# Kernel tuning notes

Hardware: AMD Instinct MI355X
Metric: run time of the kernel (lower is better)

Reference implementation:

```python
import jax, jax.numpy as jnp
import numpy as np

N, E, C, H = 20000, 100000, 32, 4
DH = C // H            # per-head dim (8x0e)
NB = 16                # num_basis_radial
HID = 64               # radial MLP hidden
WN = C * 1 * C         # FCTP weight numel: 32x0e (x) 1x0e -> 32x0e = 1024


def setup_inputs() -> dict:
    key = jax.random.key(0)
    ks = jax.random.split(key, 16)
    return {
        "node_features": jax.random.normal(ks[0], (N, C), jnp.float32),
        "edge_index": jax.random.randint(ks[1], (2, E), 0, N),
        "edge_sh": jax.random.normal(ks[2], (E, 1), jnp.float32),
        "edge_radial_emb": jax.random.uniform(ks[3], (E, NB), dtype=jnp.float32),
        "edge_length": jax.random.uniform(ks[4], (E, 1), dtype=jnp.float32),
        "max_radius": 1,
        # e3nn Linear / TP internal weights are N(0,1); fan-in scaling applied in forward
        "w_q": jax.random.normal(ks[5], (C, C), jnp.float32),
        "fck_w1": jax.random.normal(ks[6], (NB, HID), jnp.float32) / np.sqrt(NB),
        "fck_b1": jnp.zeros((HID,), jnp.float32),
        "fck_w2": jax.random.normal(ks[7], (HID, WN), jnp.float32) / np.sqrt(HID),
        "fck_b2": jnp.zeros((WN,), jnp.float32),
        "fcv_w1": jax.random.normal(ks[8], (NB, HID), jnp.float32) / np.sqrt(NB),
        "fcv_b1": jnp.zeros((HID,), jnp.float32),
        "fcv_w2": jax.random.normal(ks[9], (HID, WN), jnp.float32) / np.sqrt(HID),
        "fcv_b2": jnp.zeros((WN,), jnp.float32),
        "w_dot": jax.random.normal(ks[10], (DH, DH), jnp.float32),
        "w_out": jax.random.normal(ks[11], (C, C), jnp.float32),
        "ffn_w1": jax.random.normal(ks[12], (C, 2 * C), jnp.float32),
        "ffn_w2": jax.random.normal(ks[13], (2 * C, C), jnp.float32),
    }


def _radial(x, w1, b1, w2, b2):
    # RadialMLP: Linear -> SiLU -> Linear
    return jax.nn.silu(x @ w1 + b1) @ w2 + b2


def reference(node_features, edge_index, edge_sh, edge_radial_emb, edge_length,
              max_radius, w_q, fck_w1, fck_b1, fck_w2, fck_b2,
              fcv_w1, fcv_b1, fcv_w2, fcv_b2, w_dot, w_out, ffn_w1, ffn_w2):
    n = node_features.shape[0]
    e = edge_index.shape[1]
    src, dst = edge_index[0], edge_index[1]

    # query projection (e3nn Linear: weight / sqrt(fan_in))
    q = (node_features @ w_q) / np.sqrt(C)                       # (N, C)

    # edge K/V: radial-MLP-weighted fully-connected TP on scalar irreps
    x_src = node_features[src] * edge_sh                         # (E, C); sh is 1x0e
    kw = _radial(edge_radial_emb, fck_w1, fck_b1, fck_w2, fck_b2).reshape(e, C, C)
    vw = _radial(edge_radial_emb, fcv_w1, fcv_b1, fcv_w2, fcv_b2).reshape(e, C, C)
    tp_norm = 1.0 / np.sqrt(C * 1)                               # e3nn path normalization
    k_edge = jnp.einsum('ei,eik->ek', x_src, kw) * tp_norm       # (E, C)
    v_edge = jnp.einsum('ei,eik->ek', x_src, vw) * tp_norm       # (E, C)

    q_h = q.reshape(n, H, DH)[dst]                               # (E, H, DH)
    k_h = k_edge.reshape(e, H, DH)
    v_h = v_edge.reshape(e, H, DH)

    # per-head dot-product TP -> scalar; single module shared across heads
    dot_norm = 1.0 / np.sqrt(DH * DH)
    scale = 1.0 / np.sqrt(DH)
    logits = jnp.einsum('ehi,ehj,ij->eh', q_h, k_h, w_dot) * (dot_norm * scale)

    # soft radial cutoff multiplies the logits
    cutoff = jax.nn.sigmoid(10.0 * (1.0 - edge_length[:, 0] / max_radius))
    logits = logits * cutoff[:, None]

    # scatter-softmax over incoming edges per destination node
    m = jax.ops.segment_max(logits, dst, num_segments=n)         # (N, H)
    exl = jnp.exp(logits - m[dst])
    den = jax.ops.segment_sum(exl, dst, num_segments=n)
    attn = exl / den[dst]                                        # (E, H)

    agg = jax.ops.segment_sum(v_h * attn[..., None], dst, num_segments=n)  # (N,H,DH)
    out = (agg.reshape(n, C) @ w_out) / np.sqrt(C)

    attn_out = node_features + out                               # identity skip (in==out irreps)

    # FFN: Linear -> NormActivation(silu) -> Linear; for scalars: x*silu(|x|)/|x| = x*sigmoid(|x|)
    h = (attn_out @ ffn_w1) / np.sqrt(C)
    h = h * jax.nn.sigmoid(jnp.abs(h))
    ffn = (h @ ffn_w2) / np.sqrt(2 * C)

    return attn_out + ffn
```

## Files before the change

kernel.cpp:

```cpp
#include <hip/hip_runtime.h>
#include <hip/hip_bf16.h>
#include <hip/hip_fp16.h>
#include <math.h>

#define NNODE 20000
#define NEDGE 100000

typedef _Float16 f16x8 __attribute__((ext_vector_type(8)));
typedef float floatx16 __attribute__((ext_vector_type(16)));

#define OFF_FLAG 0
#define OFF_NF   64
#define OFF_SH   640064
#define OFF_CUT  740064
#define OFF_WQ   840064
#define OFF_WDOT 841088
#define OFF_WOUT 841152
#define OFF_FF1  842176
#define OFF_FF2  844224
#define OFF_BSWK 846272
#define OFF_BSWV 879040
#define OFF_BW1  911808
#define OFF_V16  912832
#define OFF_K16  2512832
#define OFF_HEAD 4112832
#define OFF_NEXT 4272832

#define RSQRT32 0.17677669529663687f
#define DOTSC   0.04419417382415922f

__device__ __forceinline__ float bf2f(unsigned short u) {
    return __uint_as_float(((unsigned)u) << 16);
}
__device__ __forceinline__ unsigned short f2h(float f) {
    return __builtin_bit_cast(unsigned short, (_Float16)f);
}
__device__ __forceinline__ _Float16 h2f16(unsigned short u) {
    return __builtin_bit_cast(_Float16, u);
}
__device__ __forceinline__ float silu(float s) {
    return s / (1.f + __expf(-s));
}

__device__ __forceinline__ unsigned detect_flag(const unsigned short* nf16) {
    __shared__ int cnt;
    if (threadIdx.x == 0) cnt = 0;
    __syncthreads();
    int c = 0;
    for (int r = 0; r < 2; ++r) {
        float v = bf2f(nf16[threadIdx.x + 256 * r]);
        float a = fabsf(v);
        if (a >= 2.44140625e-4f && a <= 32.0f) c++;
    }
    atomicAdd(&cnt, c);
    __syncthreads();
    return (cnt >= 400) ? 1u : 0u;
}

__device__ __forceinline__ float4 cvt4(const void* src, int i4, unsigned flag) {
    if (flag) {
        const uint2 u = ((const uint2*)src)[i4];
        return float4{bf2f((unsigned short)(u.x & 0xffffu)),
                      bf2f((unsigned short)(u.x >> 16)),
                      bf2f((unsigned short)(u.y & 0xffffu)),
                      bf2f((unsigned short)(u.y >> 16))};
    }
    return ((const float4*)src)[i4];
}

#define CSEG(cnt, off, srcp)                                                  \
    if (i < (cnt)) {                                                          \
        ws[(off) + i] = flag ? bf2f(((const unsigned short*)(srcp))[i])       \
                             : ((const float*)(srcp))[i];                     \
        return;                                                               \
    }                                                                         \
    i -= (cnt);

__global__ __launch_bounds__(256) void k_setup(float* __restrict__ ws,
    const void* nf, const void* sh, const void* len,
    const void* wq, const void* fk1, const void* fv1,
    const void* wdot, const void* wout, const void* ff1, const void* ff2,
    const void* fk2r, const void* fv2r) {
    const unsigned flag = detect_flag((const unsigned short*)nf);
    if (blockIdx.x == 0 && threadIdx.x == 0) ((unsigned*)ws)[0] = flag;
    int i = blockIdx.x * 256 + threadIdx.x;
    if (i < 160000) {
        ((float4*)(ws + OFF_NF))[i] = cvt4(nf, i, flag);
        return;
    }
    i -= 160000;
    if (i < 25000) {
        ((float4*)(ws + OFF_SH))[i] = cvt4(sh, i, flag);
        return;
    }
    i -= 25000;
    if (i < 25000) {
        const float4 L = cvt4(len, i, flag);
        float4 o;
        o.x = 1.f / (1.f + __expf(-10.f * (1.f - L.x)));
        o.y = 1.f / (1.f + __expf(-10.f * (1.f - L.y)));
        o.z = 1.f / (1.f + __expf(-10.f * (1.f - L.z)));
        o.w = 1.f / (1.f + __expf(-10.f * (1.f - L.w)));
        ((float4*)(ws + OFF_CUT))[i] = o;
        return;
    }
    i -= 25000;
    if (i < 40000) {
        ((int4*)((int*)ws + OFF_HEAD))[i] = int4{-1, -1, -1, -1};
        return;
    }
    i -= 40000;
    CSEG(1024, OFF_WQ,   wq)
    CSEG(64,   OFF_WDOT, wdot)
    CSEG(1024, OFF_WOUT, wout)
    CSEG(2048, OFF_FF1,  ff1)
    CSEG(2048, OFF_FF2,  ff2)
    if (i < 16384) {
        const int mlp = i >> 13, rem = i & 8191;
        const int s = rem >> 6, l = rem & 63;
        const int j = s >> 1, hf = s & 1;
        const void* w2 = mlp ? fv2r : fk2r;
        unsigned short o[8];
#pragma unroll
        for (int jj = 0; jj < 8; ++jj) {
            const int ii = hf * 16 + ((l >> 5) << 3) + jj;
            const int idx = j * 1024 + ii * 32 + (l & 31);
            const float vv = flag ? bf2f(((const unsigned short*)w2)[idx])
                                  : ((const float*)w2)[idx];
            o[jj] = f2h(vv * RSQRT32);
        }
        uint4 u;
        u.x = (unsigned)o[0] | ((unsigned)o[1] << 16);
        u.y = (unsigned)o[2] | ((unsigned)o[3] << 16);
        u.z = (unsigned)o[4] | ((unsigned)o[5] << 16);
        u.w = (unsigned)o[6] | ((unsigned)o[7] << 16);
        ((uint4*)(ws + (mlp ? OFF_BSWV : OFF_BSWK)))[s * 64 + l] = u;
        return;
    }
    i -= 16384;
    if (i < 256) {
        const int frag = i >> 6, l = i & 63;
        const int mlp = frag >> 1, nt = frag & 1;
        const void* w1 = mlp ? fv1 : fk1;
        unsigned short o[8];
#pragma unroll
        for (int jj = 0; jj < 8; ++jj) {
            const int k = ((l >> 5) << 3) + jj;
            const int idx = k * 64 + nt * 32 + (l & 31);
            const float vv = flag ? bf2f(((const unsigned short*)w1)[idx])
                                  : ((const float*)w1)[idx];
            o[jj] = f2h(vv);
        }
        uint4 u;
        u.x = (unsigned)o[0] | ((unsigned)o[1] << 16);
        u.y = (unsigned)o[2] | ((unsigned)o[3] << 16);
        u.z = (unsigned)o[4] | ((unsigned)o[5] << 16);
        u.w = (unsigned)o[6] | ((unsigned)o[7] << 16);
        ((uint4*)(ws + OFF_BW1))[frag * 64 + l] = u;
    }
}

__global__ __launch_bounds__(256, 3) void k_main(
    const float* __restrict__ ws, const void* __restrict__ emb_raw,
    const int* __restrict__ src, const int* __restrict__ dst,
    _Float16* __restrict__ v16, _Float16* __restrict__ k16,
    int* __restrict__ head, int* __restrict__ nxt) {
    __shared__ __align__(16) unsigned hw[128 * 66];
    const unsigned flag = ((const unsigned*)ws)[0];
    const int t = threadIdx.x;
    const int ebb = blockIdx.x * 128;

    if (t < 128) {
        const int e = ebb + t;
        if (e < NEDGE) nxt[e] = atomicExch(head + dst[e] * 8 + (e & 7), e);
    }

    const int w = t >> 6, lane = t & 63;
    const int hi = lane >> 5;

    {
        int ea = ebb + w * 32 + (lane & 31); if (ea >= NEDGE) ea = NEDGE - 1;
        f16x8 embA;
        if (flag) {
            const uint4 u = ((const uint4*)emb_raw)[ea * 2 + hi];
            const unsigned uu[4] = {u.x, u.y, u.z, u.w};
#pragma unroll
            for (int q = 0; q < 4; ++q) {
                embA[2 * q]     = (_Float16)bf2f((unsigned short)(uu[q] & 0xffffu));
                embA[2 * q + 1] = (_Float16)bf2f((unsigned short)(uu[q] >> 16));
            }
        } else {
            const float4* p = (const float4*)emb_raw + ea * 4 + hi * 2;
            const float4 a = p[0], b = p[1];
            embA[0] = (_Float16)a.x; embA[1] = (_Float16)a.y;
            embA[2] = (_Float16)a.z; embA[3] = (_Float16)a.w;
            embA[4] = (_Float16)b.x; embA[5] = (_Float16)b.y;
            embA[6] = (_Float16)b.z; embA[7] = (_Float16)b.w;
        }
        const uint4* bw1 = (const uint4*)(ws + OFF_BW1);
        const f16x8 bk0 = __builtin_bit_cast(f16x8, bw1[0 * 64 + lane]);
        const f16x8 bk1 = __builtin_bit_cast(f16x8, bw1[1 * 64 + lane]);
        const f16x8 bv0 = __builtin_bit_cast(f16x8, bw1[2 * 64 + lane]);
        const f16x8 bv1 = __builtin_bit_cast(f16x8, bw1[3 * 64 + lane]);
        floatx16 hk0 = {}, hk1 = {}, hv0 = {}, hv1 = {};
        hk0 = __builtin_amdgcn_mfma_f32_32x32x16_f16(embA, bk0, hk0, 0, 0, 0);
        hk1 = __builtin_amdgcn_mfma_f32_32x32x16_f16(embA, bk1, hk1, 0, 0, 0);
        hv0 = __builtin_amdgcn_mfma_f32_32x32x16_f16(embA, bv0, hv0, 0, 0, 0);
        hv1 = __builtin_amdgcn_mfma_f32_32x32x16_f16(embA, bv1, hv1, 0, 0, 0);
        const int colj = lane & 31;
#pragma unroll
        for (int r = 0; r < 16; ++r) {
            const int el = w * 32 + ((r & 3) + 8 * (r >> 2) + 4 * hi);
            hw[el * 66 + colj] =
                (unsigned)f2h(silu(hk0[r])) | ((unsigned)f2h(silu(hv0[r])) << 16);
            hw[el * 66 + 32 + colj] =
                (unsigned)f2h(silu(hk1[r])) | ((unsigned)f2h(silu(hv1[r])) << 16);
        }
    }

    const int kv = w & 1, grp = w >> 1;
    const int row = lane & 31;

    f16x8 xh[2][2];
#pragma unroll
    for (int rt = 0; rt < 2; ++rt) {
        int er = ebb + grp * 64 + rt * 32 + row; if (er >= NEDGE) er = NEDGE - 1;
        const int sn = src[er];
        const float shv = (ws + OFF_SH)[er];
        const float4* np = (const float4*)(ws + OFF_NF + sn * 32);
#pragma unroll
        for (int hf = 0; hf < 2; ++hf) {
            float4 a = np[hf * 4 + hi * 2];
            float4 b = np[hf * 4 + hi * 2 + 1];
            f16x8 x;
            x[0] = (_Float16)(a.x * shv); x[1] = (_Float16)(a.y * shv);
            x[2] = (_Float16)(a.z * shv); x[3] = (_Float16)(a.w * shv);
            x[4] = (_Float16)(b.x * shv); x[5] = (_Float16)(b.y * shv);
            x[6] = (_Float16)(b.z * shv); x[7] = (_Float16)(b.w * shv);
            xh[rt][hf] = x;
        }
    }
    __syncthreads();

    const unsigned* hb0 = hw + (grp * 64 + row) * 66;
    const unsigned* hb1 = hb0 + 32 * 66;
    const uint4* bg = (const uint4*)(ws + (kv ? OFF_BSWV : OFF_BSWK));
    floatx16 a0 = {}, a1 = {};
    const int c0 = w * 4;

#define LOADB(cc, B, H0, H1)                                                  \
    {                                                                         \
        const int c_ = (cc) & 15;                                             \
        _Pragma("unroll")                                                     \
        for (int q = 0; q < 8; ++q) B[q] = bg[(c_ * 8 + q) * 64 + lane];      \
        _Pragma("unroll")                                                     \
        for (int jl = 0; jl < 4; ++jl) {                                      \
            H0[jl] = hb0[c_ * 4 + jl];                                        \
            H1[jl] = hb1[c_ * 4 + jl];                                        \
        }                                                                     \
    }

#define DOMFMA(B, H0, H1)                                                     \
    {                                                                         \
        _Pragma("unroll")                                                     \
        for (int jl = 0; jl < 4; ++jl) {                                      \
            const unsigned h0 = H0[jl], h1 = H1[jl];                          \
            const _Float16 hr0 =                                              \
                h2f16((unsigned short)(kv ? (h0 >> 16) : (h0 & 0xffffu)));    \
            const _Float16 hr1 =                                              \
                h2f16((unsigned short)(kv ? (h1 >> 16) : (h1 & 0xffffu)));    \
            _Pragma("unroll")                                                 \
            for (int hf = 0; hf < 2; ++hf) {                                  \
                const f16x8 b = __builtin_bit_cast(f16x8, B[jl * 2 + hf]);    \
                a0 = __builtin_amdgcn_mfma_f32_32x32x16_f16(                  \
                    xh[0][hf] * hr0, b, a0, 0, 0, 0);                         \
                a1 = __builtin_amdgcn_mfma_f32_32x32x16_f16(                  \
                    xh[1][hf] * hr1, b, a1, 0, 0, 0);                         \
            }                                                                 \
        }                                                                     \
    }

    {
        uint4 bA[8], bB[8];
        unsigned hA0[4], hA1[4], hB0[4], hB1[4];
        LOADB(c0, bA, hA0, hA1);
#pragma unroll
        for (int s = 0; s < 8; ++s) {
            LOADB(c0 + 2 * s + 1, bB, hB0, hB1);
            DOMFMA(bA, hA0, hA1);
            if (s < 7) LOADB(c0 + 2 * s + 2, bA, hA0, hA1);
            DOMFMA(bB, hB0, hB1);
        }
    }
#undef LOADB
#undef DOMFMA

    _Float16* outp = kv ? v16 : k16;
    const int col = lane & 31;
#pragma unroll
    for (int rt = 0; rt < 2; ++rt) {
        const floatx16 ar = rt ? a1 : a0;
#pragma unroll
        for (int r = 0; r < 16; ++r) {
            const int rowe = (r & 3) + 8 * (r >> 2) + 4 * hi;
            const int e = ebb + grp * 64 + rt * 32 + rowe;
            if (e < NEDGE) outp[e * 32 + col] = (_Float16)ar[r];
        }
    }
}

__global__ __launch_bounds__(256) void k_final(const float* __restrict__ ws,
                                               void* __restrict__ out) {
    __shared__ float wqd[1024];
    __shared__ float s1[8][33];
    __shared__ float s_q[8][33];
    __shared__ float h_s[8][65];
    const int t = threadIdx.x, nl = t >> 5, c = t & 31, h = c >> 3;
    const int n = blockIdx.x * 8 + nl;
    const unsigned flag = ((const unsigned*)ws)[0];
    const float* cutp = ws + OFF_CUT;
    const float* wout = ws + OFF_WOUT;
    const float* ff1  = ws + OFF_FF1;
    const float* ff2  = ws + OFF_FF2;
    const _Float16* v16 = (const _Float16*)(ws + OFF_V16);
    const _Float16* k16 = (const _Float16*)(ws + OFF_K16);
    const int* headp = (const int*)ws + OFF_HEAD;
    const int* nxt   = (const int*)ws + OFF_NEXT;

    const float nfv = (ws + OFF_NF)[n * 32 + c];

    {
        const float* wqp = ws + OFF_WQ;
        const float* wd  = ws + OFF_WDOT;
        const int m0 = t >> 5, ch = t & 31, hh = ch >> 3, jx = ch & 7;
#pragma unroll
        for (int r = 0; r < 4; ++r) {
            const int m = r * 8 + m0;
            float s = 0.f;
#pragma unroll
            for (int i = 0; i < 8; ++i)
                s = fmaf(wqp[m * 32 + hh * 8 + i], wd[i * 8 + jx], s);
            wqd[m * 32 + ch] = s;
        }
    }
    s1[nl][c] = nfv;
    __syncthreads();
    {
        float s = 0.f;
#pragma unroll
        for (int m = 0; m < 32; ++m) s = fmaf(s1[nl][m], wqd[m * 32 + c], s);
        s_q[nl][c] = s * (RSQRT32 * DOTSC);
    }
    __syncthreads();

    const float q0 = s_q[nl][h * 8 + 0], q1 = s_q[nl][h * 8 + 1];
    const float q2 = s_q[nl][h * 8 + 2], q3 = s_q[nl][h * 8 + 3];
    const float q4 = s_q[nl][h * 8 + 4], q5 = s_q[nl][h * 8 + 5];
    const float q6 = s_q[nl][h * 8 + 6], q7 = s_q[nl][h * 8 + 7];

    float mm[8], dd[8], aa[8];
    int pp[8];
#pragma unroll
    for (int ch = 0; ch < 8; ++ch) {
        mm[ch] = -1e30f; dd[ch] = 0.f; aa[ch] = 0.f;
        pp[ch] = headp[8 * n + ch];
    }
    for (;;) {
        bool any = false;
#pragma unroll
        for (int ch = 0; ch < 8; ++ch) any = any || (pp[ch] >= 0);
        if (!any) break;
#pragma unroll
        for (int ch = 0; ch < 8; ++ch) {
            const int e = pp[ch];
            if (e >= 0) {
                const f16x8 kk = __builtin_bit_cast(f16x8, *(const uint4*)(k16 + e * 32 + h * 8));
                float lg = q0 * (float)kk[0] + q1 * (float)kk[1] + q2 * (float)kk[2]
                         + q3 * (float)kk[3] + q4 * (float)kk[4] + q5 * (float)kk[5]
                         + q6 * (float)kk[6] + q7 * (float)kk[7];
                lg *= cutp[e];
                const float vv = (float)v16[e * 32 + c];
                const float mn = fmaxf(mm[ch], lg);
                const float sc = __expf(mm[ch] - mn), wgt = __expf(lg - mn);
                dd[ch] = dd[ch] * sc + wgt;
                aa[ch] = aa[ch] * sc + wgt * vv;
                mm[ch] = mn;
                pp[ch] = nxt[e];
            }
        }
    }
    float mn = mm[0];
#pragma unroll
    for (int ch = 1; ch < 8; ++ch) mn = fmaxf(mn, mm[ch]);
    float dn = 0.f, acc = 0.f;
#pragma unroll
    for (int ch = 0; ch < 8; ++ch) {
        const float sc = __expf(mm[ch] - mn);
        dn += dd[ch] * sc;
        acc += aa[ch] * sc;
    }
    const float ao_in = dn > 0.f ? acc / dn : 0.f;
    __syncthreads();
    s1[nl][c] = ao_in;
    __syncthreads();
    float o = 0.f;
#pragma unroll
    for (int i2 = 0; i2 < 32; ++i2) o = fmaf(s1[nl][i2], wout[i2 * 32 + c], o);
    const float ao = nfv + o * RSQRT32;
    __syncthreads();
    s1[nl][c] = ao;
    __syncthreads();
#pragma unroll
    for (int r = 0; r < 2; ++r) {
        const int cc = c + r * 32;
        float z = 0.f;
#pragma unroll
        for (int i2 = 0; i2 < 32; ++i2) z = fmaf(s1[nl][i2], ff1[i2 * 64 + cc], z);
        z *= RSQRT32;
        z = z / (1.f + __expf(-fabsf(z)));
        h_s[nl][cc] = z;
    }
    __syncthreads();
    float f = 0.f;
#pragma unroll
    for (int i2 = 0; i2 < 64; ++i2) f = fmaf(h_s[nl][i2], ff2[i2 * 32 + c], f);
    const float fin = ao + f * 0.125f;
    if (flag) ((__hip_bfloat16*)out)[n * 32 + c] = __float2bfloat16(fin);
    else      ((float*)out)[n * 32 + c] = fin;
}

extern "C" void kernel_launch(void* const* d_in, const int* in_sizes, int n_in,
                              void* d_out, int out_size, void* d_ws, size_t ws_size,
                              hipStream_t stream) {
    (void)in_sizes; (void)n_in; (void)out_size; (void)ws_size;
    float* ws = (float*)d_ws;
    const int* eidx = (const int*)d_in[1];
    const int* src = eidx;
    const int* dst = eidx + NEDGE;

    k_setup<<<1066, 256, 0, stream>>>(ws,
        d_in[0], d_in[2], d_in[4], d_in[6], d_in[7], d_in[11],
        d_in[15], d_in[16], d_in[17], d_in[18], d_in[9], d_in[13]);
    k_main<<<(NEDGE + 127) / 128, 256, 0, stream>>>(ws, d_in[3], src, dst,
        (_Float16*)(ws + OFF_V16), (_Float16*)(ws + OFF_K16),
        (int*)ws + OFF_HEAD, (int*)ws + OFF_NEXT);
    k_final<<<NNODE / 8, 256, 0, stream>>>(ws, d_out);
}
```

Baseline: 169.3 us.

## Halve edges per block in k_main and replicate swizzled FCTP weights 8x

k_main now handles 64 edges per block instead of 128. Each wave does one 32-row MFMA tile instead of two, the LDS hidden buffer is halved, and launch bounds allow 4 blocks per CU. The swizzled K/V second-layer weights are written as 8 replicas in the workspace, and each block reads the replica chosen by blockIdx&7, to spread load contention on the shared weight table. The cost is that each weight fetch now serves half as many edges, so total weight traffic per edge doubles. Only two of the four waves run the radial first-layer MFMA, and k_setup does 8x more stores.

```diff
diff --git a/kernel.cpp b/kernel.cpp
--- a/kernel.cpp
+++ b/kernel.cpp
@@ -25,6 +25,7 @@
 #define OFF_K16  2512832
 #define OFF_HEAD 4112832
 #define OFF_NEXT 4272832
+#define OFF_BREP 4372832
 
 #define RSQRT32 0.17677669529663687f
 #define DOTSC   0.04419417382415922f
@@ -134,7 +135,10 @@
         u.y = (unsigned)o[2] | ((unsigned)o[3] << 16);
         u.z = (unsigned)o[4] | ((unsigned)o[5] << 16);
         u.w = (unsigned)o[6] | ((unsigned)o[7] << 16);
-        ((uint4*)(ws + (mlp ? OFF_BSWV : OFF_BSWK)))[s * 64 + l] = u;
+        uint4* rep = (uint4*)(ws + OFF_BREP);
+        const int idx4 = (mlp ? 8192 : 0) + s * 64 + l;
+#pragma unroll
+        for (int x = 0; x < 8; ++x) rep[x * 16384 + idx4] = u;
         return;
     }
     i -= 16384;
@@ -160,17 +164,17 @@
     }
 }
 
-__global__ __launch_bounds__(256, 3) void k_main(
+__global__ __launch_bounds__(256, 4) void k_main(
     const float* __restrict__ ws, const void* __restrict__ emb_raw,
     const int* __restrict__ src, const int* __restrict__ dst,
     _Float16* __restrict__ v16, _Float16* __restrict__ k16,
     int* __restrict__ head, int* __restrict__ nxt) {
-    __shared__ __align__(16) unsigned hw[128 * 66];
+    __shared__ __align__(16) unsigned hw[64 * 66];
     const unsigned flag = ((const unsigned*)ws)[0];
     const int t = threadIdx.x;
-    const int ebb = blockIdx.x * 128;
-
-    if (t < 128) {
+    const int ebb = blockIdx.x * 64;
+
+    if (t < 64) {
         const int e = ebb + t;
         if (e < NEDGE) nxt[e] = atomicExch(head + dst[e] * 8 + (e & 7), e);
     }
@@ -178,7 +182,7 @@
     const int w = t >> 6, lane = t & 63;
     const int hi = lane >> 5;
 
-    {
+    if (w < 2) {
         int ea = ebb + w * 32 + (lane & 31); if (ea >= NEDGE) ea = NEDGE - 1;
         f16x8 embA;
         if (flag) {
@@ -221,10 +225,9 @@
     const int kv = w & 1, grp = w >> 1;
     const int row = lane & 31;
 
-    f16x8 xh[2][2];
-#pragma unroll
-    for (int rt = 0; rt < 2; ++rt) {
-        int er = ebb + grp * 64 + rt * 32 + row; if (er >= NEDGE) er = NEDGE - 1;
+    f16x8 xh[2];
+    {
+        int er = ebb + grp * 32 + row; if (er >= NEDGE) er = NEDGE - 1;
         const int sn = src[er];
         const float shv = (ws + OFF_SH)[er];
         const float4* np = (const float4*)(ws + OFF_NF + sn * 32);
@@ -237,59 +240,52 @@
             x[2] = (_Float16)(a.z * shv); x[3] = (_Float16)(a.w * shv);
             x[4] = (_Float16)(b.x * shv); x[5] = (_Float16)(b.y * shv);
             x[6] = (_Float16)(b.z * shv); x[7] = (_Float16)(b.w * shv);
-            xh[rt][hf] = x;
-        }
-    }
-    __syncthreads();
-
-    const unsigned* hb0 = hw + (grp * 64 + row) * 66;
-    const unsigned* hb1 = hb0 + 32 * 66;
-    const uint4* bg = (const uint4*)(ws + (kv ? OFF_BSWV : OFF_BSWK));
-    floatx16 a0 = {}, a1 = {};
+            xh[hf] = x;
+        }
+    }
+    __syncthreads();
+
+    const unsigned* hb0 = hw + (grp * 32 + row) * 66;
+    const uint4* bg = (const uint4*)(ws + OFF_BREP)
+                    + (blockIdx.x & 7) * 16384 + (kv ? 8192 : 0);
+    floatx16 a0 = {};
     const int c0 = w * 4;
 
-#define LOADB(cc, B, H0, H1)                                                  \
+#define LOADB(cc, B, H0)                                                      \
     {                                                                         \
         const int c_ = (cc) & 15;                                             \
         _Pragma("unroll")                                                     \
         for (int q = 0; q < 8; ++q) B[q] = bg[(c_ * 8 + q) * 64 + lane];      \
         _Pragma("unroll")                                                     \
-        for (int jl = 0; jl < 4; ++jl) {                                      \
-            H0[jl] = hb0[c_ * 4 + jl];                                        \
-            H1[jl] = hb1[c_ * 4 + jl];                                        \
-        }                                                                     \
-    }
-
-#define DOMFMA(B, H0, H1)                                                     \
+        for (int jl = 0; jl < 4; ++jl) H0[jl] = hb0[c_ * 4 + jl];             \
+    }
+
+#define DOMFMA(B, H0)                                                         \
     {                                                                         \
         _Pragma("unroll")                                                     \
         for (int jl = 0; jl < 4; ++jl) {                                      \
-            const unsigned h0 = H0[jl], h1 = H1[jl];                          \
+            const unsigned h0 = H0[jl];                                       \
             const _Float16 hr0 =                                              \
                 h2f16((unsigned short)(kv ? (h0 >> 16) : (h0 & 0xffffu)));    \
-            const _Float16 hr1 =                                              \
-                h2f16((unsigned short)(kv ? (h1 >> 16) : (h1 & 0xffffu)));    \
             _Pragma("unroll")                                                 \
             for (int hf = 0; hf < 2; ++hf) {                                  \
                 const f16x8 b = __builtin_bit_cast(f16x8, B[jl * 2 + hf]);    \
                 a0 = __builtin_amdgcn_mfma_f32_32x32x16_f16(                  \
-                    xh[0][hf] * hr0, b, a0, 0, 0, 0);                         \
-                a1 = __builtin_amdgcn_mfma_f32_32x32x16_f16(                  \
-                    xh[1][hf] * hr1, b, a1, 0, 0, 0);                         \
+                    xh[hf] * hr0, b, a0, 0, 0, 0);                            \
             }                                                                 \
         }                                                                     \
     }
 
     {
         uint4 bA[8], bB[8];
-        unsigned hA0[4], hA1[4], hB0[4], hB1[4];
-        LOADB(c0, bA, hA0, hA1);
+        unsigned hA0[4], hB0[4];
+        LOADB(c0, bA, hA0);
 #pragma unroll
         for (int s = 0; s < 8; ++s) {
-            LOADB(c0 + 2 * s + 1, bB, hB0, hB1);
-            DOMFMA(bA, hA0, hA1);
-            if (s < 7) LOADB(c0 + 2 * s + 2, bA, hA0, hA1);
-            DOMFMA(bB, hB0, hB1);
+            LOADB(c0 + 2 * s + 1, bB, hB0);
+            DOMFMA(bA, hA0);
+            if (s < 7) LOADB(c0 + 2 * s + 2, bA, hA0);
+            DOMFMA(bB, hB0);
         }
     }
 #undef LOADB
@@ -298,14 +294,10 @@
     _Float16* outp = kv ? v16 : k16;
     const int col = lane & 31;
 #pragma unroll
-    for (int rt = 0; rt < 2; ++rt) {
-        const floatx16 ar = rt ? a1 : a0;
-#pragma unroll
-        for (int r = 0; r < 16; ++r) {
-            const int rowe = (r & 3) + 8 * (r >> 2) + 4 * hi;
-            const int e = ebb + grp * 64 + rt * 32 + rowe;
-            if (e < NEDGE) outp[e * 32 + col] = (_Float16)ar[r];
-        }
+    for (int r = 0; r < 16; ++r) {
+        const int rowe = (r & 3) + 8 * (r >> 2) + 4 * hi;
+        const int e = ebb + grp * 32 + rowe;
+        if (e < NEDGE) outp[e * 32 + col] = (_Float16)a0[r];
     }
 }
 
@@ -441,7 +433,7 @@
     k_setup<<<1066, 256, 0, stream>>>(ws,
         d_in[0], d_in[2], d_in[4], d_in[6], d_in[7], d_in[11],
         d_in[15], d_in[16], d_in[17], d_in[18], d_in[9], d_in[13]);
-    k_main<<<(NEDGE + 127) / 128, 256, 0, stream>>>(ws, d_in[3], src, dst,
+    k_main<<<(NEDGE + 63) / 64, 256, 0, stream>>>(ws, d_in[3], src, dst,
         (_Float16*)(ws + OFF_V16), (_Float16*)(ws + OFF_K16),
         (int*)ws + OFF_HEAD, (int*)ws + OFF_NEXT);
     k_final<<<NNODE / 8, 256, 0, stream>>>(ws, d_out);
```

New measurement: 173.5 us. 2.5% more time.

## Replicate swizzled MLP weights 8x and split MFMA accumulators to break dependency chains

Applied to the files above, without the earlier changes.

The prep kernel now writes eight copies of the swizzled second-layer radial weights, and each main block reads the copy selected by its block index. This is meant to spread the L2/channel traffic from all blocks loading the same weight lines. The MFMA loop also uses four independent accumulators instead of two, which shortens the dependency chains between back-to-back MFMAs, and the partial sums are added at the end. The cost is more accumulator registers, so launch bounds drop from 3 to 2 blocks per SM, plus extra workspace and extra replicated writes during prep.

```diff
diff --git a/kernel.cpp b/kernel.cpp
--- a/kernel.cpp
+++ b/kernel.cpp
@@ -25,6 +25,7 @@
 #define OFF_K16  2512832
 #define OFF_HEAD 4112832
 #define OFF_NEXT 4272832
+#define OFF_BREP 4372832
 
 #define RSQRT32 0.17677669529663687f
 #define DOTSC   0.04419417382415922f
@@ -134,7 +135,10 @@
         u.y = (unsigned)o[2] | ((unsigned)o[3] << 16);
         u.z = (unsigned)o[4] | ((unsigned)o[5] << 16);
         u.w = (unsigned)o[6] | ((unsigned)o[7] << 16);
-        ((uint4*)(ws + (mlp ? OFF_BSWV : OFF_BSWK)))[s * 64 + l] = u;
+        uint4* rep = (uint4*)(ws + OFF_BREP);
+        const int idx4 = (mlp ? 8192 : 0) + s * 64 + l;
+#pragma unroll
+        for (int x = 0; x < 8; ++x) rep[x * 16384 + idx4] = u;
         return;
     }
     i -= 16384;
@@ -160,7 +164,7 @@
     }
 }
 
-__global__ __launch_bounds__(256, 3) void k_main(
+__global__ __launch_bounds__(256, 2) void k_main(
     const float* __restrict__ ws, const void* __restrict__ emb_raw,
     const int* __restrict__ src, const int* __restrict__ dst,
     _Float16* __restrict__ v16, _Float16* __restrict__ k16,
@@ -244,8 +248,9 @@
 
     const unsigned* hb0 = hw + (grp * 64 + row) * 66;
     const unsigned* hb1 = hb0 + 32 * 66;
-    const uint4* bg = (const uint4*)(ws + (kv ? OFF_BSWV : OFF_BSWK));
-    floatx16 a0 = {}, a1 = {};
+    const uint4* bg = (const uint4*)(ws + OFF_BREP)
+                    + (blockIdx.x & 7) * 16384 + (kv ? 8192 : 0);
+    floatx16 a00 = {}, a01 = {}, a10 = {}, a11 = {};
     const int c0 = w * 4;
 
 #define LOADB(cc, B, H0, H1)                                                  \
@@ -269,14 +274,16 @@
                 h2f16((unsigned short)(kv ? (h0 >> 16) : (h0 & 0xffffu)));    \
             const _Float16 hr1 =                                              \
                 h2f16((unsigned short)(kv ? (h1 >> 16) : (h1 & 0xffffu)));    \
-            _Pragma("unroll")                                                 \
-            for (int hf = 0; hf < 2; ++hf) {                                  \
-                const f16x8 b = __builtin_bit_cast(f16x8, B[jl * 2 + hf]);    \
-                a0 = __builtin_amdgcn_mfma_f32_32x32x16_f16(                  \
-                    xh[0][hf] * hr0, b, a0, 0, 0, 0);                         \
-                a1 = __builtin_amdgcn_mfma_f32_32x32x16_f16(                  \
-                    xh[1][hf] * hr1, b, a1, 0, 0, 0);                         \
-            }                                                                 \
+            const f16x8 b0 = __builtin_bit_cast(f16x8, B[jl * 2 + 0]);        \
+            const f16x8 b1 = __builtin_bit_cast(f16x8, B[jl * 2 + 1]);        \
+            a00 = __builtin_amdgcn_mfma_f32_32x32x16_f16(                     \
+                xh[0][0] * hr0, b0, a00, 0, 0, 0);                            \
+            a10 = __builtin_amdgcn_mfma_f32_32x32x16_f16(                     \
+                xh[1][0] * hr1, b0, a10, 0, 0, 0);                            \
+            a01 = __builtin_amdgcn_mfma_f32_32x32x16_f16(                     \
+                xh[0][1] * hr0, b1, a01, 0, 0, 0);                            \
+            a11 = __builtin_amdgcn_mfma_f32_32x32x16_f16(                     \
+                xh[1][1] * hr1, b1, a11, 0, 0, 0);                            \
         }                                                                     \
     }
 
@@ -297,9 +304,10 @@
 
     _Float16* outp = kv ? v16 : k16;
     const int col = lane & 31;
+    const floatx16 accr[2] = {a00 + a01, a10 + a11};
 #pragma unroll
     for (int rt = 0; rt < 2; ++rt) {
-        const floatx16 ar = rt ? a1 : a0;
+        const floatx16 ar = accr[rt];
 #pragma unroll
         for (int r = 0; r < 16; ++r) {
             const int rowe = (r & 3) + 8 * (r >> 2) + 4 * hi;
```

Measured after the change: 172.3 us. About the same (+1.8%).

## Precompute query projection in setup and drop max-subtraction in softmax

Applied to the files above, without the earlier changes.

The query projection (node features times the fused w_q·w_dot matrix) moves out of k_final into extra threads of k_setup, which write a per-node q buffer to the workspace. Each k_final block no longer rebuilds the 32x32 fused weight in shared memory. The per-edge online softmax is replaced by a plain sum of exp(logit) with no running max, cutting one exp and the rescaling per edge. The risks are exp overflow for large logits, and redundant fused-weight recomputation in every setup thread.

```diff
diff --git a/kernel.cpp b/kernel.cpp
--- a/kernel.cpp
+++ b/kernel.cpp
@@ -13,8 +13,6 @@
 #define OFF_NF   64
 #define OFF_SH   640064
 #define OFF_CUT  740064
-#define OFF_WQ   840064
-#define OFF_WDOT 841088
 #define OFF_WOUT 841152
 #define OFF_FF1  842176
 #define OFF_FF2  844224
@@ -25,6 +23,7 @@
 #define OFF_K16  2512832
 #define OFF_HEAD 4112832
 #define OFF_NEXT 4272832
+#define OFF_Q    4372832
 
 #define RSQRT32 0.17677669529663687f
 #define DOTSC   0.04419417382415922f
@@ -55,6 +54,10 @@
     atomicAdd(&cnt, c);
     __syncthreads();
     return (cnt >= 400) ? 1u : 0u;
+}
+
+__device__ __forceinline__ float rdf(const void* p, int idx, unsigned flag) {
+    return flag ? bf2f(((const unsigned short*)p)[idx]) : ((const float*)p)[idx];
 }
 
 __device__ __forceinline__ float4 cvt4(const void* src, int i4, unsigned flag) {
@@ -70,8 +73,7 @@
 
 #define CSEG(cnt, off, srcp)                                                  \
     if (i < (cnt)) {                                                          \
-        ws[(off) + i] = flag ? bf2f(((const unsigned short*)(srcp))[i])       \
-                             : ((const float*)(srcp))[i];                     \
+        ws[(off) + i] = rdf(srcp, i, flag);                                   \
         return;                                                               \
     }                                                                         \
     i -= (cnt);
@@ -110,8 +112,29 @@
         return;
     }
     i -= 40000;
-    CSEG(1024, OFF_WQ,   wq)
-    CSEG(64,   OFF_WDOT, wdot)
+    if (i < 160000) {
+        const int c = i & 31, nb = i >> 5;
+        const int h = c >> 3, jx = c & 7;
+        float wqdc[32];
+        for (int m = 0; m < 32; ++m) {
+            float s = 0.f;
+#pragma unroll
+            for (int ii = 0; ii < 8; ++ii)
+                s = fmaf(rdf(wq, m * 32 + h * 8 + ii, flag),
+                         rdf(wdot, ii * 8 + jx, flag), s);
+            wqdc[m] = s;
+        }
+#pragma unroll
+        for (int nn = 0; nn < 4; ++nn) {
+            const int n = nb * 4 + nn;
+            float s = 0.f;
+            for (int m = 0; m < 32; ++m)
+                s = fmaf(rdf(nf, n * 32 + m, flag), wqdc[m], s);
+            ws[OFF_Q + n * 32 + c] = s * (RSQRT32 * DOTSC);
+        }
+        return;
+    }
+    i -= 160000;
     CSEG(1024, OFF_WOUT, wout)
     CSEG(2048, OFF_FF1,  ff1)
     CSEG(2048, OFF_FF2,  ff2)
@@ -125,9 +148,7 @@
         for (int jj = 0; jj < 8; ++jj) {
             const int ii = hf * 16 + ((l >> 5) << 3) + jj;
             const int idx = j * 1024 + ii * 32 + (l & 31);
-            const float vv = flag ? bf2f(((const unsigned short*)w2)[idx])
-                                  : ((const float*)w2)[idx];
-            o[jj] = f2h(vv * RSQRT32);
+            o[jj] = f2h(rdf(w2, idx, flag) * RSQRT32);
         }
         uint4 u;
         u.x = (unsigned)o[0] | ((unsigned)o[1] << 16);
@@ -146,10 +167,7 @@
 #pragma unroll
         for (int jj = 0; jj < 8; ++jj) {
             const int k = ((l >> 5) << 3) + jj;
-            const int idx = k * 64 + nt * 32 + (l & 31);
-            const float vv = flag ? bf2f(((const unsigned short*)w1)[idx])
-                                  : ((const float*)w1)[idx];
-            o[jj] = f2h(vv);
+            o[jj] = f2h(rdf(w1, k * 64 + nt * 32 + (l & 31), flag));
         }
         uint4 u;
         u.x = (unsigned)o[0] | ((unsigned)o[1] << 16);
@@ -311,7 +329,6 @@
 
 __global__ __launch_bounds__(256) void k_final(const float* __restrict__ ws,
                                                void* __restrict__ out) {
-    __shared__ float wqd[1024];
     __shared__ float s1[8][33];
     __shared__ float s_q[8][33];
     __shared__ float h_s[8][65];
@@ -328,29 +345,7 @@
     const int* nxt   = (const int*)ws + OFF_NEXT;
 
     const float nfv = (ws + OFF_NF)[n * 32 + c];
-
-    {
-        const float* wqp = ws + OFF_WQ;
-        const float* wd  = ws + OFF_WDOT;
-        const int m0 = t >> 5, ch = t & 31, hh = ch >> 3, jx = ch & 7;
-#pragma unroll
-        for (int r = 0; r < 4; ++r) {
-            const int m = r * 8 + m0;
-            float s = 0.f;
-#pragma unroll
-            for (int i = 0; i < 8; ++i)
-                s = fmaf(wqp[m * 32 + hh * 8 + i], wd[i * 8 + jx], s);
-            wqd[m * 32 + ch] = s;
-        }
-    }
-    s1[nl][c] = nfv;
-    __syncthreads();
-    {
-        float s = 0.f;
-#pragma unroll
-        for (int m = 0; m < 32; ++m) s = fmaf(s1[nl][m], wqd[m * 32 + c], s);
-        s_q[nl][c] = s * (RSQRT32 * DOTSC);
-    }
+    s_q[nl][c] = (ws + OFF_Q)[n * 32 + c];
     __syncthreads();
 
     const float q0 = s_q[nl][h * 8 + 0], q1 = s_q[nl][h * 8 + 1];
@@ -358,11 +353,11 @@
     const float q4 = s_q[nl][h * 8 + 4], q5 = s_q[nl][h * 8 + 5];
     const float q6 = s_q[nl][h * 8 + 6], q7 = s_q[nl][h * 8 + 7];
 
-    float mm[8], dd[8], aa[8];
+    float dd[8], aa[8];
     int pp[8];
 #pragma unroll
     for (int ch = 0; ch < 8; ++ch) {
-        mm[ch] = -1e30f; dd[ch] = 0.f; aa[ch] = 0.f;
+        dd[ch] = 0.f; aa[ch] = 0.f;
         pp[ch] = headp[8 * n + ch];
     }
     for (;;) {
@@ -378,27 +373,17 @@
                 float lg = q0 * (float)kk[0] + q1 * (float)kk[1] + q2 * (float)kk[2]
                          + q3 * (float)kk[3] + q4 * (float)kk[4] + q5 * (float)kk[5]
                          + q6 * (float)kk[6] + q7 * (float)kk[7];
-                lg *= cutp[e];
+                const float wgt = __expf(lg * cutp[e]);
                 const float vv = (float)v16[e * 32 + c];
-                const float mn = fmaxf(mm[ch], lg);
-                const float sc = __expf(mm[ch] - mn), wgt = __expf(lg - mn);
-                dd[ch] = dd[ch] * sc + wgt;
-                aa[ch] = aa[ch] * sc + wgt * vv;
-                mm[ch] = mn;
+                dd[ch] += wgt;
+                aa[ch] += wgt * vv;
                 pp[ch] = nxt[e];
             }
         }
     }
-    float mn = mm[0];
-#pragma unroll
-    for (int ch = 1; ch < 8; ++ch) mn = fmaxf(mn, mm[ch]);
     float dn = 0.f, acc = 0.f;
 #pragma unroll
-    for (int ch = 0; ch < 8; ++ch) {
-        const float sc = __expf(mm[ch] - mn);
-        dn += dd[ch] * sc;
-        acc += aa[ch] * sc;
-    }
+    for (int ch = 0; ch < 8; ++ch) { dn += dd[ch]; acc += aa[ch]; }
     const float ao_in = dn > 0.f ? acc / dn : 0.f;
     __syncthreads();
     s1[nl][c] = ao_in;
@@ -438,7 +423,7 @@
     const int* src = eidx;
     const int* dst = eidx + NEDGE;
 
-    k_setup<<<1066, 256, 0, stream>>>(ws,
+    k_setup<<<1687, 256, 0, stream>>>(ws,
         d_in[0], d_in[2], d_in[4], d_in[6], d_in[7], d_in[11],
         d_in[15], d_in[16], d_in[17], d_in[18], d_in[9], d_in[13]);
     k_main<<<(NEDGE + 127) / 128, 256, 0, stream>>>(ws, d_in[3], src, dst,
```

Result: slower. 199.8 us (+18.0%).
